# Kernel tuning notes

Measured on AMD Instinct MI355X. Metric: run time of the kernel, lower is better.

The kernel has to match this reference:

```python
import jax, jax.numpy as jnp
import numpy as np

# index_map: new group -> list of old column indices (covers 23 old classes -> 10 groups)
INDEX_MAP = {0: [0, 1], 1: [2, 3], 2: [4, 5, 6], 3: [7, 8], 4: [9, 10, 11],
             5: [12, 13], 6: [14, 15, 16], 7: [17, 18], 8: [19, 20], 9: [21, 22]}
C_OLD = 23
G = len(INDEX_MAP)

# Membership matrix M[c, g] = 1 if old column c belongs to group g.
# outputs[:, g] = sum_{c in group g} inputs[:, c]  ==  inputs @ M
_M_np = np.zeros((C_OLD, G), dtype=np.float32)
for g, olds in INDEX_MAP.items():
    for c in olds:
        _M_np[c, g] = 1.0

B, N = 8, 262144


def setup_inputs() -> dict:
    key = jax.random.key(0)
    k1, k2 = jax.random.split(key)
    inputs = jax.random.uniform(k1, (B, N, C_OLD), dtype=jnp.float32)  # positive logits/scores
    t = jax.random.uniform(k2, (B, G), dtype=jnp.float32)
    targets = t / jnp.sum(t, axis=-1, keepdims=True)  # probability targets for KLDiv
    return {"inputs": inputs, "targets": targets}


def reference(inputs, targets):
    M = jnp.asarray(_M_np)                                 # [C, G]
    # grouped scatter-sum over columns (the nested loops in the original)
    outputs = jnp.einsum('bnc,cg->bng', inputs, M)         # [B, N, G]
    probs = outputs / jnp.sum(outputs, axis=-1, keepdims=True)
    avg_probs = jnp.mean(probs, axis=1)                    # [B, G]
    log_avg = jnp.log(avg_probs)
    # KLDivLoss(reduction='batchmean') on a 1-D input of length G divides by G:
    # loss_b = sum_g t[g] * (log t[g] - log_avg[g]) / G
    kl_per_b = jnp.sum(targets * (jnp.log(targets) - log_avg), axis=-1) / G
    return jnp.mean(kl_per_b)
```

## Files before the change

### kernel.cpp

```cpp
#include <hip/hip_runtime.h>
#include <math.h>

#define C_OLD 23
#define G 10
#define BVAL 8
#define NVAL 262144
#define BLOCK 256
#define ROWS_PER_TILE 256
#define TILES 8
#define BLOCKS_PER_B 128
#define TILE_FLOATS (ROWS_PER_TILE * C_OLD)
#define TILE_VEC4   (TILE_FLOATS / 4)
#define FULL_VEC_ITERS (TILE_VEC4 / BLOCK)

__global__ __launch_bounds__(BLOCK) void group_prob_partial_kernel(
        const float* __restrict__ in, float* __restrict__ part) {
    __shared__ float tile[TILE_FLOATS];
    __shared__ float wpart[BLOCK / 64][G];

    const int tid = threadIdx.x;
    const int b   = blockIdx.x / BLOCKS_PER_B;
    const int blk = blockIdx.x % BLOCKS_PER_B;
    const long long rowBase = (long long)b * NVAL
                            + (long long)blk * (ROWS_PER_TILE * TILES);

    float acc[G];
    #pragma unroll
    for (int g = 0; g < G; ++g) acc[g] = 0.0f;

    for (int t = 0; t < TILES; ++t) {
        const float4* __restrict__ src =
            (const float4*)(in + (rowBase + (long long)t * ROWS_PER_TILE) * C_OLD);
        float4* dst = (float4*)tile;
        #pragma unroll
        for (int i = 0; i < FULL_VEC_ITERS; ++i)
            dst[tid + i * BLOCK] = src[tid + i * BLOCK];
        if (tid < TILE_VEC4 - FULL_VEC_ITERS * BLOCK)
            dst[tid + FULL_VEC_ITERS * BLOCK] = src[tid + FULL_VEC_ITERS * BLOCK];
        __syncthreads();

        const float* row = tile + tid * C_OLD;
        float s0 = row[0] + row[1];
        float s1 = row[2] + row[3];
        float s2 = row[4] + row[5] + row[6];
        float s3 = row[7] + row[8];
        float s4 = row[9] + row[10] + row[11];
        float s5 = row[12] + row[13];
        float s6 = row[14] + row[15] + row[16];
        float s7 = row[17] + row[18];
        float s8 = row[19] + row[20];
        float s9 = row[21] + row[22];
        float tot = ((s0 + s1) + (s2 + s3)) + ((s4 + s5) + (s6 + s7)) + (s8 + s9);
        float inv = 1.0f / tot;
        acc[0] += s0 * inv; acc[1] += s1 * inv; acc[2] += s2 * inv;
        acc[3] += s3 * inv; acc[4] += s4 * inv; acc[5] += s5 * inv;
        acc[6] += s6 * inv; acc[7] += s7 * inv; acc[8] += s8 * inv;
        acc[9] += s9 * inv;
        __syncthreads();
    }

    #pragma unroll
    for (int g = 0; g < G; ++g) {
        float v = acc[g];
        #pragma unroll
        for (int off = 32; off > 0; off >>= 1)
            v += __shfl_down(v, off, 64);
        acc[g] = v;
    }
    const int wave = tid >> 6;
    const int lane = tid & 63;
    if (lane == 0) {
        #pragma unroll
        for (int g = 0; g < G; ++g) wpart[wave][g] = acc[g];
    }
    __syncthreads();
    if (tid < G) {
        float s = wpart[0][tid] + wpart[1][tid] + wpart[2][tid] + wpart[3][tid];
        part[((long long)b * G + tid) * BLOCKS_PER_B + blk] = s;
    }
}

__global__ void finalize_kernel(const float* __restrict__ part,
                                const float* __restrict__ tgt,
                                float* __restrict__ out) {
    __shared__ double red[128];
    const int t = threadIdx.x;
    double term = 0.0;
    if (t < BVAL * G) {
        double s = 0.0;
        const float* p = part + (long long)t * BLOCKS_PER_B;
        #pragma unroll 8
        for (int i = 0; i < BLOCKS_PER_B; ++i) s += (double)p[i];
        double avg = s / (double)NVAL;
        double tv  = (double)tgt[t];
        term = tv * (log(tv) - log(avg));
    }
    red[t] = term;
    __syncthreads();
    #pragma unroll
    for (int s = 64; s > 0; s >>= 1) {
        if (t < s) red[t] += red[t + s];
        __syncthreads();
    }
    if (t == 0) out[0] = (float)(red[0] / (double)(G * BVAL));
}

extern "C" void kernel_launch(void* const* d_in, const int* in_sizes, int n_in,
                              void* d_out, int out_size, void* d_ws, size_t ws_size,
                              hipStream_t stream) {
    const float* inputs  = (const float*)d_in[0];
    const float* targets = (const float*)d_in[1];
    float* out  = (float*)d_out;
    float* part = (float*)d_ws;

    group_prob_partial_kernel<<<BVAL * BLOCKS_PER_B, BLOCK, 0, stream>>>(inputs, part);
    finalize_kernel<<<1, 128, 0, stream>>>(part, targets, out);
}
```

Measured before the change: 270.0 us.

## Register-prefetch next tile and fuse finalize via last-block atomic counter

```diff
diff --git a/kernel.cpp b/kernel.cpp
--- a/kernel.cpp
+++ b/kernel.cpp
@@ -9,14 +9,21 @@
 #define ROWS_PER_TILE 256
 #define TILES 8
 #define BLOCKS_PER_B 128
+#define NBLOCKS (BVAL * BLOCKS_PER_B)
 #define TILE_FLOATS (ROWS_PER_TILE * C_OLD)
 #define TILE_VEC4   (TILE_FLOATS / 4)
-#define FULL_VEC_ITERS (TILE_VEC4 / BLOCK)
+#define REM_VEC4    (TILE_VEC4 - 5 * BLOCK)
 
-__global__ __launch_bounds__(BLOCK) void group_prob_partial_kernel(
-        const float* __restrict__ in, float* __restrict__ part) {
+#define COUNTER_OFF 40960
+
+__global__ __launch_bounds__(BLOCK) void grouped_kl_kernel(
+        const float* __restrict__ in, const float* __restrict__ tgt,
+        float* __restrict__ part, unsigned int* __restrict__ counter,
+        float* __restrict__ out) {
     __shared__ float tile[TILE_FLOATS];
     __shared__ float wpart[BLOCK / 64][G];
+    __shared__ unsigned int isLast;
+    __shared__ double red[128];
 
     const int tid = threadIdx.x;
     const int b   = blockIdx.x / BLOCKS_PER_B;
@@ -28,16 +35,31 @@
     #pragma unroll
     for (int g = 0; g < G; ++g) acc[g] = 0.0f;
 
+    float4 r0, r1, r2, r3, r4, r5;
+    float4* dstv = (float4*)tile;
+
+    {
+        const float4* src = (const float4*)(in + rowBase * C_OLD);
+        r0 = src[tid];              r1 = src[tid + 1 * BLOCK];
+        r2 = src[tid + 2 * BLOCK];  r3 = src[tid + 3 * BLOCK];
+        r4 = src[tid + 4 * BLOCK];
+        if (tid < REM_VEC4) r5 = src[tid + 5 * BLOCK];
+        dstv[tid] = r0;             dstv[tid + 1 * BLOCK] = r1;
+        dstv[tid + 2 * BLOCK] = r2; dstv[tid + 3 * BLOCK] = r3;
+        dstv[tid + 4 * BLOCK] = r4;
+        if (tid < REM_VEC4) dstv[tid + 5 * BLOCK] = r5;
+    }
+    __syncthreads();
+
     for (int t = 0; t < TILES; ++t) {
-        const float4* __restrict__ src =
-            (const float4*)(in + (rowBase + (long long)t * ROWS_PER_TILE) * C_OLD);
-        float4* dst = (float4*)tile;
-        #pragma unroll
-        for (int i = 0; i < FULL_VEC_ITERS; ++i)
-            dst[tid + i * BLOCK] = src[tid + i * BLOCK];
-        if (tid < TILE_VEC4 - FULL_VEC_ITERS * BLOCK)
-            dst[tid + FULL_VEC_ITERS * BLOCK] = src[tid + FULL_VEC_ITERS * BLOCK];
-        __syncthreads();
+        if (t + 1 < TILES) {
+            const float4* src = (const float4*)(
+                in + (rowBase + (long long)(t + 1) * ROWS_PER_TILE) * C_OLD);
+            r0 = src[tid];              r1 = src[tid + 1 * BLOCK];
+            r2 = src[tid + 2 * BLOCK];  r3 = src[tid + 3 * BLOCK];
+            r4 = src[tid + 4 * BLOCK];
+            if (tid < REM_VEC4) r5 = src[tid + 5 * BLOCK];
+        }
 
         const float* row = tile + tid * C_OLD;
         float s0 = row[0] + row[1];
@@ -57,6 +79,14 @@
         acc[6] += s6 * inv; acc[7] += s7 * inv; acc[8] += s8 * inv;
         acc[9] += s9 * inv;
         __syncthreads();
+
+        if (t + 1 < TILES) {
+            dstv[tid] = r0;             dstv[tid + 1 * BLOCK] = r1;
+            dstv[tid + 2 * BLOCK] = r2; dstv[tid + 3 * BLOCK] = r3;
+            dstv[tid + 4 * BLOCK] = r4;
+            if (tid < REM_VEC4) dstv[tid + 5 * BLOCK] = r5;
+            __syncthreads();
+        }
     }
 
     #pragma unroll
@@ -78,31 +108,37 @@
         float s = wpart[0][tid] + wpart[1][tid] + wpart[2][tid] + wpart[3][tid];
         part[((long long)b * G + tid) * BLOCKS_PER_B + blk] = s;
     }
-}
 
-__global__ void finalize_kernel(const float* __restrict__ part,
-                                const float* __restrict__ tgt,
-                                float* __restrict__ out) {
-    __shared__ double red[128];
-    const int t = threadIdx.x;
+    __threadfence();
+    if (tid == 0) {
+        unsigned int old = atomicAdd(counter, 1u);
+        isLast = (old == NBLOCKS - 1) ? 1u : 0u;
+    }
+    __syncthreads();
+    if (!isLast) return;
+    __threadfence();
+
     double term = 0.0;
-    if (t < BVAL * G) {
+    if (tid < BVAL * G) {
+        const float4* p4 = (const float4*)(part + (long long)tid * BLOCKS_PER_B);
         double s = 0.0;
-        const float* p = part + (long long)t * BLOCKS_PER_B;
         #pragma unroll 8
-        for (int i = 0; i < BLOCKS_PER_B; ++i) s += (double)p[i];
+        for (int i = 0; i < BLOCKS_PER_B / 4; ++i) {
+            float4 v = p4[i];
+            s += (double)v.x + (double)v.y + (double)v.z + (double)v.w;
+        }
         double avg = s / (double)NVAL;
-        double tv  = (double)tgt[t];
+        double tv  = (double)tgt[tid];
         term = tv * (log(tv) - log(avg));
     }
-    red[t] = term;
+    if (tid < 128) red[tid] = term;
     __syncthreads();
     #pragma unroll
     for (int s = 64; s > 0; s >>= 1) {
-        if (t < s) red[t] += red[t + s];
+        if (tid < s) red[tid] += red[tid + s];
         __syncthreads();
     }
-    if (t == 0) out[0] = (float)(red[0] / (double)(G * BVAL));
+    if (tid == 0) out[0] = (float)(red[0] / (double)(G * BVAL));
 }
 
 extern "C" void kernel_launch(void* const* d_in, const int* in_sizes, int n_in,
@@ -112,7 +148,8 @@
     const float* targets = (const float*)d_in[1];
     float* out  = (float*)d_out;
     float* part = (float*)d_ws;
+    unsigned int* counter = (unsigned int*)((char*)d_ws + COUNTER_OFF);
 
-    group_prob_partial_kernel<<<BVAL * BLOCKS_PER_B, BLOCK, 0, stream>>>(inputs, part);
-    finalize_kernel<<<1, 128, 0, stream>>>(part, targets, out);
+    hipMemsetAsync(counter, 0, sizeof(unsigned int), stream);
+    grouped_kl_kernel<<<NBLOCKS, BLOCK, 0, stream>>>(inputs, targets, part, counter, out);
 }
```

Result: slower. 431.5 us (+59.8%).

## Stage input per wave with register prefetch and drop block-wide barriers

Applied to the files above, without the earlier changes.

```diff
diff --git a/kernel.cpp b/kernel.cpp
--- a/kernel.cpp
+++ b/kernel.cpp
@@ -6,40 +6,57 @@
 #define BVAL 8
 #define NVAL 262144
 #define BLOCK 256
-#define ROWS_PER_TILE 256
-#define TILES 8
+#define WAVES (BLOCK / 64)
+#define ROWS_PER_CHUNK 64
+#define CHUNKS 8
 #define BLOCKS_PER_B 128
-#define TILE_FLOATS (ROWS_PER_TILE * C_OLD)
-#define TILE_VEC4   (TILE_FLOATS / 4)
-#define FULL_VEC_ITERS (TILE_VEC4 / BLOCK)
+#define NBLOCKS (BVAL * BLOCKS_PER_B)
+#define CHUNK_FLOATS (ROWS_PER_CHUNK * C_OLD)
+#define CHUNK_VEC4 (CHUNK_FLOATS / 4)
 
 __global__ __launch_bounds__(BLOCK) void group_prob_partial_kernel(
         const float* __restrict__ in, float* __restrict__ part) {
-    __shared__ float tile[TILE_FLOATS];
-    __shared__ float wpart[BLOCK / 64][G];
+    __shared__ float lds[WAVES][CHUNK_FLOATS];
+    __shared__ float wpart[WAVES][G];
 
-    const int tid = threadIdx.x;
-    const int b   = blockIdx.x / BLOCKS_PER_B;
-    const int blk = blockIdx.x % BLOCKS_PER_B;
+    const int tid  = threadIdx.x;
+    const int wave = tid >> 6;
+    const int lane = tid & 63;
+    const int b    = blockIdx.x >> 7;
+    const int blk  = blockIdx.x & (BLOCKS_PER_B - 1);
+
     const long long rowBase = (long long)b * NVAL
-                            + (long long)blk * (ROWS_PER_TILE * TILES);
+                            + (long long)blk * (ROWS_PER_CHUNK * CHUNKS * WAVES)
+                            + (long long)wave * (ROWS_PER_CHUNK * CHUNKS);
+    const float4* __restrict__ src0 = (const float4*)(in + rowBase * C_OLD);
+
+    float4* dstv = (float4*)lds[wave];
+    const float* row = lds[wave] + lane * C_OLD;
 
     float acc[G];
     #pragma unroll
     for (int g = 0; g < G; ++g) acc[g] = 0.0f;
 
-    for (int t = 0; t < TILES; ++t) {
-        const float4* __restrict__ src =
-            (const float4*)(in + (rowBase + (long long)t * ROWS_PER_TILE) * C_OLD);
-        float4* dst = (float4*)tile;
-        #pragma unroll
-        for (int i = 0; i < FULL_VEC_ITERS; ++i)
-            dst[tid + i * BLOCK] = src[tid + i * BLOCK];
-        if (tid < TILE_VEC4 - FULL_VEC_ITERS * BLOCK)
-            dst[tid + FULL_VEC_ITERS * BLOCK] = src[tid + FULL_VEC_ITERS * BLOCK];
-        __syncthreads();
+    float4 r0, r1, r2, r3, r4, r5;
 
-        const float* row = tile + tid * C_OLD;
+    {
+        const float4* s = src0;
+        r0 = s[lane];        r1 = s[lane + 64];   r2 = s[lane + 128];
+        r3 = s[lane + 192];  r4 = s[lane + 256];
+        if (lane < CHUNK_VEC4 - 320) r5 = s[lane + 320];
+        dstv[lane] = r0;         dstv[lane + 64] = r1;   dstv[lane + 128] = r2;
+        dstv[lane + 192] = r3;   dstv[lane + 256] = r4;
+        if (lane < CHUNK_VEC4 - 320) dstv[lane + 320] = r5;
+    }
+
+    for (int c = 0; c < CHUNKS; ++c) {
+        if (c + 1 < CHUNKS) {
+            const float4* s = src0 + (c + 1) * CHUNK_VEC4;
+            r0 = s[lane];        r1 = s[lane + 64];   r2 = s[lane + 128];
+            r3 = s[lane + 192];  r4 = s[lane + 256];
+            if (lane < CHUNK_VEC4 - 320) r5 = s[lane + 320];
+        }
+
         float s0 = row[0] + row[1];
         float s1 = row[2] + row[3];
         float s2 = row[4] + row[5] + row[6];
@@ -56,7 +73,12 @@
         acc[3] += s3 * inv; acc[4] += s4 * inv; acc[5] += s5 * inv;
         acc[6] += s6 * inv; acc[7] += s7 * inv; acc[8] += s8 * inv;
         acc[9] += s9 * inv;
-        __syncthreads();
+
+        if (c + 1 < CHUNKS) {
+            dstv[lane] = r0;         dstv[lane + 64] = r1;   dstv[lane + 128] = r2;
+            dstv[lane + 192] = r3;   dstv[lane + 256] = r4;
+            if (lane < CHUNK_VEC4 - 320) dstv[lane + 320] = r5;
+        }
     }
 
     #pragma unroll
@@ -67,8 +89,6 @@
             v += __shfl_down(v, off, 64);
         acc[g] = v;
     }
-    const int wave = tid >> 6;
-    const int lane = tid & 63;
     if (lane == 0) {
         #pragma unroll
         for (int g = 0; g < G; ++g) wpart[wave][g] = acc[g];
@@ -87,10 +107,13 @@
     const int t = threadIdx.x;
     double term = 0.0;
     if (t < BVAL * G) {
+        const float4* p4 = (const float4*)(part + (long long)t * BLOCKS_PER_B);
         double s = 0.0;
-        const float* p = part + (long long)t * BLOCKS_PER_B;
         #pragma unroll 8
-        for (int i = 0; i < BLOCKS_PER_B; ++i) s += (double)p[i];
+        for (int i = 0; i < BLOCKS_PER_B / 4; ++i) {
+            float4 v = p4[i];
+            s += (double)v.x + (double)v.y + (double)v.z + (double)v.w;
+        }
         double avg = s / (double)NVAL;
         double tv  = (double)tgt[t];
         term = tv * (log(tv) - log(avg));
@@ -113,6 +136,6 @@
     float* out  = (float*)d_out;
     float* part = (float*)d_ws;
 
-    group_prob_partial_kernel<<<BVAL * BLOCKS_PER_B, BLOCK, 0, stream>>>(inputs, part);
+    group_prob_partial_kernel<<<NBLOCKS, BLOCK, 0, stream>>>(inputs, part);
     finalize_kernel<<<1, 128, 0, stream>>>(part, targets, out);
 }
```

After: 267.8 us. No clear change (-0.8%).
